# Optimization experiments

Hardware: AMD Instinct MI355X
Metric: run time of the kernel (lower is better)

## Reference

```python
import jax, jax.numpy as jnp
import numpy as np

B, IN, H, OUT, E = 8192, 1024, 4096, 1024, 8
HG = H // 2  # gating hidden

def setup_inputs() -> dict:
    key = jax.random.key(0)
    ks = jax.random.split(key, 9)
    s_in = 1.0 / np.sqrt(IN)
    s_h = 1.0 / np.sqrt(H)
    s_hg = 1.0 / np.sqrt(HG)
    return {
        "x": jax.random.normal(ks[0], (B, IN), jnp.float32),
        # gating MLP: Linear(IN,HG) -> ReLU -> Linear(HG,E) -> softmax
        "gw1": jax.random.uniform(ks[1], (IN, HG), jnp.float32, -s_in, s_in),
        "gb1": jax.random.uniform(ks[2], (HG,), jnp.float32, -s_in, s_in),
        "gw2": jax.random.uniform(ks[3], (HG, E), jnp.float32, -s_hg, s_hg),
        "gb2": jax.random.uniform(ks[4], (E,), jnp.float32, -s_hg, s_hg),
        # experts: E x (Linear(IN,H) -> ReLU -> Linear(H,OUT))
        "ew1": jax.random.uniform(ks[5], (E, IN, H), jnp.float32, -s_in, s_in),
        "eb1": jax.random.uniform(ks[6], (E, H), jnp.float32, -s_in, s_in),
        "ew2": jax.random.uniform(ks[7], (E, H, OUT), jnp.float32, -s_h, s_h),
        "eb2": jax.random.uniform(ks[8], (E, OUT), jnp.float32, -s_h, s_h),
    }

def reference(x, gw1, gb1, gw2, gb2, ew1, eb1, ew2, eb2):
    # Gating network (dropout is a no-op in eval)
    gh = jax.nn.relu(x @ gw1 + gb1)                       # [B, HG]
    gates = jax.nn.softmax(gh @ gw2 + gb2, axis=1)        # [B, E]
    # All experts run on the full batch
    h = jax.nn.relu(jnp.einsum('bi,eih->beh', x, ew1) + eb1[None])  # [B, E, H]
    eo = jnp.einsum('beh,eho->beo', h, ew2) + eb2[None]             # [B, E, OUT]
    # Gate-weighted combine: (stacked * gates[...,None]).sum(dim=1)
    combined = jnp.einsum('beo,be->bo', eo, gates)        # [B, OUT]
    return combined
```

## Files before the change

### kernel.cpp

```cpp
#include <hip/hip_runtime.h>


#define DI __device__ __forceinline__

typedef _Float16 f16;
typedef _Float16 f16x8 __attribute__((ext_vector_type(8)));
typedef float f32x4 __attribute__((ext_vector_type(4)));

constexpr int BSZ  = 8192;
constexpr int IND  = 1024;
constexpr int HID  = 4096;
constexpr int OUTD = 1024;
constexpr int NE   = 8;
constexpr int HGD  = 2048;

__global__ __launch_bounds__(256) void conv_f32_f16_kernel(
    const float* __restrict__ in, f16* __restrict__ out)
{
    size_t i = ((size_t)blockIdx.x * 256 + threadIdx.x) * 8;
    const float4* p = (const float4*)(in + i);
    float4 a = p[0], b = p[1];
    f16x8 v = {(f16)a.x, (f16)a.y, (f16)a.z, (f16)a.w,
               (f16)b.x, (f16)b.y, (f16)b.z, (f16)b.w};
    *(f16x8*)(out + i) = v;
}

__global__ __launch_bounds__(256) void transpose_f32_f16_kernel(
    const float* __restrict__ W, f16* __restrict__ Wt, int K, int N)
{
    __shared__ float t[64][65];
    int n0 = blockIdx.x * 64, k0 = blockIdx.y * 64;
    int tx = threadIdx.x & 63, ty = threadIdx.x >> 6;
#pragma unroll
    for (int i = 0; i < 16; i++) {
        int k = i * 4 + ty;
        t[k][tx] = W[(size_t)(k0 + k) * N + n0 + tx];
    }
    __syncthreads();
#pragma unroll
    for (int i = 0; i < 16; i++) {
        int n = i * 4 + ty;
        Wt[(size_t)(n0 + n) * K + k0 + tx] = (f16)t[tx][n];
    }
}

DI void gload_lds16(const void* g, void* l)
{
    typedef const __attribute__((address_space(1))) unsigned int as1_t;
    typedef __attribute__((address_space(3))) unsigned int as3_t;
    __builtin_amdgcn_global_load_lds(
        (as1_t*)(unsigned long long)(__SIZE_TYPE__)g,
        (as3_t*)(unsigned int)(__SIZE_TYPE__)l,
        16, 0, 0);
}

#define SYNC_HEAD                                                              \
    __builtin_amdgcn_sched_barrier(0);                                         \
    __builtin_amdgcn_s_barrier();                                              \
    asm volatile("s_waitcnt lgkmcnt(0)" ::: "memory");                         \
    __builtin_amdgcn_sched_barrier(0);
#define SYNC_HEAD_T8                                                           \
    __builtin_amdgcn_sched_barrier(0);                                         \
    asm volatile("s_waitcnt lgkmcnt(8)");                                      \
    __builtin_amdgcn_s_barrier();                                              \
    asm volatile("s_waitcnt lgkmcnt(0)" ::: "memory");                         \
    __builtin_amdgcn_sched_barrier(0);
#define SYNC_TAIL                                                              \
    __builtin_amdgcn_sched_barrier(0);                                         \
    __builtin_amdgcn_s_barrier();                                              \
    asm volatile("" ::: "memory");

template <bool RELU>
__global__ __launch_bounds__(512, 2) void gemm256_kernel(
    const f16* __restrict__ A, const f16* __restrict__ Bt,
    const float* __restrict__ bias, f16* __restrict__ Cptr,
    int M, int N, int K)
{
    constexpr int BM = 256, BN = 256, BK = 64;
    constexpr int AT = BM * BK * 2, BT = BN * BK * 2;
    __shared__ __align__(16) f16 sA[2][BM * BK];
    __shared__ __align__(16) f16 sB[2][BN * BK];
    const char* sAc = (const char*)sA;
    const char* sBc = (const char*)sB;

    const int tid = threadIdx.x, wid = tid >> 6, lane = tid & 63;
    const int wm = wid >> 2, wn = wid & 3;
    const int nwg = gridDim.x, bid = blockIdx.x;
    const int wg = (bid & 7) * (nwg >> 3) + (bid >> 3);
    const int gx = N / BN;
    const size_t bm = (size_t)(wg / gx) * BM;
    const size_t bn = (size_t)(wg % gx) * BN;

    f32x4 acc[8][4] = {};

    const int rho  = tid >> 3;
    const int slot = (((tid & 7) << 4) ^ (((tid >> 3) & 7) << 4));
    const f16* pA = A  + (bm + rho) * (size_t)K + (slot >> 1);
    const f16* pB = Bt + (bn + rho) * (size_t)K + (slot >> 1);

    auto stA = [&](int b, int q, int T) {
        gload_lds16(pA + ((size_t)q * 64) * K + (size_t)T * BK,
                    (char*)sAc + b * AT + q * 8192 + wid * 1024);
    };
    auto stB = [&](int b, int q, int T) {
        gload_lds16(pB + ((size_t)q * 64) * K + (size_t)T * BK,
                    (char*)sBc + b * BT + q * 8192 + wid * 1024);
    };

    int offA0[8], offB0[4];
#pragma unroll
    for (int f = 0; f < 8; f++) {
        int r = wm * 128 + f * 16 + (lane & 15);
        offA0[f] = r * 128 + ((((lane >> 4) << 4)) ^ ((r & 7) << 4));
    }
#pragma unroll
    for (int f = 0; f < 4; f++) {
        int r = wn * 64 + f * 16 + (lane & 15);
        offB0[f] = r * 128 + ((((lane >> 4) << 4)) ^ ((r & 7) << 4));
    }

    f16x8 av[4][2], bv0[2][2], bv1[2][2];

#define LDAQ(B, MH)                                                            \
    _Pragma("unroll") for (int f = 0; f < 4; f++)                              \
    _Pragma("unroll") for (int kc = 0; kc < 2; kc++)                           \
        av[f][kc] = *(const f16x8*)(sAc + (B) * AT + (offA0[(MH)*4+f] ^ (kc << 6)));
#define LDBH(B, NH, BV)                                                        \
    _Pragma("unroll") for (int f = 0; f < 2; f++)                              \
    _Pragma("unroll") for (int kc = 0; kc < 2; kc++)                           \
        BV[f][kc] = *(const f16x8*)(sBc + (B) * BT + (offB0[(NH)*2+f] ^ (kc << 6)));
#define QUAD(MH, NH, BV)                                                       \
    __builtin_amdgcn_s_setprio(1);                                             \
    _Pragma("unroll") for (int f = 0; f < 4; f++)                              \
    _Pragma("unroll") for (int g = 0; g < 2; g++)                              \
    _Pragma("unroll") for (int kc = 0; kc < 2; kc++)                           \
        acc[(MH)*4+f][(NH)*2+g] = __builtin_amdgcn_mfma_f32_16x16x32_f16(      \
            av[f][kc], BV[g][kc], acc[(MH)*4+f][(NH)*2+g], 0, 0, 0);           \
    __builtin_amdgcn_s_setprio(0);

    const int NT = K / BK, NI = NT / 2;

    stA(0,0,0); stA(0,2,0); stB(0,0,0); stB(0,1,0); stB(0,2,0); stB(0,3,0);
    stA(0,1,0); stA(0,3,0);
    stA(1,0,1); stA(1,2,1); stB(1,0,1); stB(1,1,1); stB(1,2,1); stB(1,3,1);
    asm volatile("s_waitcnt vmcnt(6)");
    __builtin_amdgcn_s_barrier();
    asm volatile("" ::: "memory");

    for (int i = 0; i < NI - 1; ++i) {
        const int t = 2 * i;
        LDAQ(0, 0) LDBH(0, 0, bv0)
        stA(1, 1, t + 1); stA(1, 3, t + 1);
        SYNC_HEAD_T8
        QUAD(0, 0, bv0)
        SYNC_TAIL
        LDBH(0, 1, bv1)
        stA(0, 0, t + 2); stA(0, 2, t + 2);
        SYNC_HEAD
        QUAD(0, 1, bv1)
        SYNC_TAIL
        LDAQ(0, 1)
        stB(0, 0, t + 2); stB(0, 1, t + 2);
        SYNC_HEAD
        QUAD(1, 1, bv1)
        SYNC_TAIL
        stB(0, 2, t + 2); stB(0, 3, t + 2);
        SYNC_HEAD
        QUAD(1, 0, bv0)
        asm volatile("s_waitcnt vmcnt(6)");
        SYNC_TAIL
        LDAQ(1, 0) LDBH(1, 0, bv0)
        stA(0, 1, t + 2); stA(0, 3, t + 2);
        SYNC_HEAD_T8
        QUAD(0, 0, bv0)
        SYNC_TAIL
        LDBH(1, 1, bv1)
        stA(1, 0, t + 3); stA(1, 2, t + 3);
        SYNC_HEAD
        QUAD(0, 1, bv1)
        SYNC_TAIL
        LDAQ(1, 1)
        stB(1, 0, t + 3); stB(1, 1, t + 3);
        SYNC_HEAD
        QUAD(1, 1, bv1)
        SYNC_TAIL
        stB(1, 2, t + 3); stB(1, 3, t + 3);
        SYNC_HEAD
        QUAD(1, 0, bv0)
        asm volatile("s_waitcnt vmcnt(6)");
        SYNC_TAIL
    }
    {
        LDAQ(0, 0) LDBH(0, 0, bv0)
        stA(1, 1, NT - 1); stA(1, 3, NT - 1);
        SYNC_HEAD_T8
        QUAD(0, 0, bv0)
        SYNC_TAIL
        LDBH(0, 1, bv1)
        SYNC_HEAD
        QUAD(0, 1, bv1)
        SYNC_TAIL
        LDAQ(0, 1)
        SYNC_HEAD
        QUAD(1, 1, bv1)
        SYNC_TAIL
        SYNC_HEAD
        QUAD(1, 0, bv0)
        asm volatile("s_waitcnt vmcnt(0)");
        SYNC_TAIL
        LDAQ(1, 0) LDBH(1, 0, bv0)
        SYNC_HEAD
        QUAD(0, 0, bv0)
        SYNC_TAIL
        LDBH(1, 1, bv1)
        SYNC_HEAD
        QUAD(0, 1, bv1)
        SYNC_TAIL
        LDAQ(1, 1)
        SYNC_HEAD
        QUAD(1, 1, bv1)
        SYNC_TAIL
        SYNC_HEAD
        QUAD(1, 0, bv0)
        SYNC_TAIL
    }
#undef LDAQ
#undef LDBH
#undef QUAD

    const size_t row0 = bm + (size_t)wm * 128;
    const int col0 = (int)bn + wn * 64;
    const int c0 = lane & 15, r0 = (lane >> 4) * 4;
#pragma unroll
    for (int fm = 0; fm < 8; fm++)
#pragma unroll
        for (int r = 0; r < 4; r++) {
            const size_t row = row0 + fm * 16 + r0 + r;
#pragma unroll
            for (int n = 0; n < 4; n++) {
                const size_t col = (size_t)col0 + n * 16 + c0;
                float v = acc[fm][n][r] + bias[col];
                if constexpr (RELU) v = fmaxf(v, 0.0f);
                Cptr[row * (size_t)N + col] = (f16)v;
            }
        }
}

template <bool ACCUM>
__global__ __launch_bounds__(512, 2) void gemmO_kernel(
    const f16* __restrict__ A, const f16* __restrict__ Bt,
    const float* __restrict__ bias, const float* __restrict__ gate,
    float* __restrict__ Cptr, int M, int N, int K)
{
    constexpr int BM = 256, BN = 128, BK = 64;
    constexpr int AT = BM * BK * 2, BT = BN * BK * 2;
    __shared__ __align__(16) f16 sA[2][BM * BK];
    __shared__ __align__(16) f16 sB[2][BN * BK];
    const char* sAc = (const char*)sA;
    const char* sBc = (const char*)sB;

    const int tid = threadIdx.x, wid = tid >> 6, lane = tid & 63;
    const int wm = wid >> 2, wn = wid & 3;
    const int nwg = gridDim.x, bid = blockIdx.x;
    const int wg = (bid & 7) * (nwg >> 3) + (bid >> 3);
    const int gx = N / BN;
    const size_t bm = (size_t)(wg / gx) * BM;
    const size_t bn = (size_t)(wg % gx) * BN;

    f32x4 acc[8][2] = {};

    const int rho  = tid >> 3;
    const int slot = (((tid & 7) << 4) ^ (((tid >> 3) & 7) << 4));
    const f16* pA = A  + (bm + rho) * (size_t)K + (slot >> 1);
    const f16* pB = Bt + (bn + rho) * (size_t)K + (slot >> 1);

    auto stA = [&](int b, int q, int T) {
        gload_lds16(pA + ((size_t)q * 64) * K + (size_t)T * BK,
                    (char*)sAc + b * AT + q * 8192 + wid * 1024);
    };
    auto stB = [&](int b, int q, int T) {
        gload_lds16(pB + ((size_t)q * 64) * K + (size_t)T * BK,
                    (char*)sBc + b * BT + q * 8192 + wid * 1024);
    };

    int offA0[8], offB0[2];
#pragma unroll
    for (int f = 0; f < 8; f++) {
        int r = wm * 128 + f * 16 + (lane & 15);
        offA0[f] = r * 128 + ((((lane >> 4) << 4)) ^ ((r & 7) << 4));
    }
#pragma unroll
    for (int f = 0; f < 2; f++) {
        int r = wn * 32 + f * 16 + (lane & 15);
        offB0[f] = r * 128 + ((((lane >> 4) << 4)) ^ ((r & 7) << 4));
    }

    f16x8 av[4], bv[2][2];

#define LDA4(B, MH, KC)                                                        \
    _Pragma("unroll") for (int f = 0; f < 4; f++)                              \
        av[f] = *(const f16x8*)(sAc + (B) * AT + (offA0[(MH)*4+f] ^ ((KC) << 6)));
#define LDBA(B)                                                                \
    _Pragma("unroll") for (int f = 0; f < 2; f++)                              \
    _Pragma("unroll") for (int kc = 0; kc < 2; kc++)                           \
        bv[f][kc] = *(const f16x8*)(sBc + (B) * BT + (offB0[f] ^ (kc << 6)));
#define OCT(MH, KC)                                                            \
    __builtin_amdgcn_s_setprio(1);                                             \
    _Pragma("unroll") for (int f = 0; f < 4; f++)                              \
    _Pragma("unroll") for (int g = 0; g < 2; g++)                              \
        acc[(MH)*4+f][g] = __builtin_amdgcn_mfma_f32_16x16x32_f16(             \
            av[f], bv[g][KC], acc[(MH)*4+f][g], 0, 0, 0);                      \
    __builtin_amdgcn_s_setprio(0);

    const int NT = K / BK, NI = NT / 2;

    stA(0,0,0); stA(0,2,0); stB(0,0,0); stB(0,1,0); stA(0,1,0); stA(0,3,0);
    stA(1,0,1); stA(1,2,1); stB(1,0,1); stB(1,1,1);
    asm volatile("s_waitcnt vmcnt(4)");
    __builtin_amdgcn_s_barrier();
    asm volatile("" ::: "memory");

    for (int i = 0; i < NI - 1; ++i) {
        const int t = 2 * i;
        LDA4(0, 0, 0) LDBA(0)
        stA(1, 1, t + 1); stA(1, 3, t + 1);
        SYNC_HEAD
        OCT(0, 0)
        SYNC_TAIL
        LDA4(0, 0, 1)
        SYNC_HEAD
        OCT(0, 1)
        SYNC_TAIL
        LDA4(0, 1, 0)
        stA(0, 0, t + 2); stA(0, 2, t + 2);
        SYNC_HEAD
        OCT(1, 0)
        SYNC_TAIL
        LDA4(0, 1, 1)
        stB(0, 0, t + 2); stB(0, 1, t + 2);
        SYNC_HEAD
        OCT(1, 1)
        asm volatile("s_waitcnt vmcnt(4)");
        SYNC_TAIL
        LDA4(1, 0, 0) LDBA(1)
        stA(0, 1, t + 2); stA(0, 3, t + 2);
        SYNC_HEAD
        OCT(0, 0)
        SYNC_TAIL
        LDA4(1, 0, 1)
        SYNC_HEAD
        OCT(0, 1)
        SYNC_TAIL
        LDA4(1, 1, 0)
        stA(1, 0, t + 3); stA(1, 2, t + 3);
        SYNC_HEAD
        OCT(1, 0)
        SYNC_TAIL
        LDA4(1, 1, 1)
        stB(1, 0, t + 3); stB(1, 1, t + 3);
        SYNC_HEAD
        OCT(1, 1)
        asm volatile("s_waitcnt vmcnt(4)");
        SYNC_TAIL
    }
    {
        LDA4(0, 0, 0) LDBA(0)
        stA(1, 1, NT - 1); stA(1, 3, NT - 1);
        SYNC_HEAD
        OCT(0, 0)
        SYNC_TAIL
        LDA4(0, 0, 1)
        SYNC_HEAD
        OCT(0, 1)
        SYNC_TAIL
        LDA4(0, 1, 0)
        SYNC_HEAD
        OCT(1, 0)
        SYNC_TAIL
        LDA4(0, 1, 1)
        SYNC_HEAD
        OCT(1, 1)
        asm volatile("s_waitcnt vmcnt(0)");
        SYNC_TAIL
        LDA4(1, 0, 0) LDBA(1)
        SYNC_HEAD
        OCT(0, 0)
        SYNC_TAIL
        LDA4(1, 0, 1)
        SYNC_HEAD
        OCT(0, 1)
        SYNC_TAIL
        LDA4(1, 1, 0)
        SYNC_HEAD
        OCT(1, 0)
        SYNC_TAIL
        LDA4(1, 1, 1)
        SYNC_HEAD
        OCT(1, 1)
        SYNC_TAIL
    }
#undef LDA4
#undef LDBA
#undef OCT

    const size_t row0 = bm + (size_t)wm * 128;
    const int col0 = (int)bn + wn * 32;
    const int c0 = lane & 15, r0 = (lane >> 4) * 4;
#pragma unroll
    for (int fm = 0; fm < 8; fm++)
#pragma unroll
        for (int r = 0; r < 4; r++) {
            const size_t row = row0 + fm * 16 + r0 + r;
            const float g = gate[row * NE];
#pragma unroll
            for (int n = 0; n < 2; n++) {
                const size_t col = (size_t)col0 + n * 16 + c0;
                float v = (acc[fm][n][r] + bias[col]) * g;
                float* p = Cptr + row * (size_t)N + col;
                *p = ACCUM ? (*p + v) : v;
            }
        }
}

__global__ __launch_bounds__(256) void gate_softmax_kernel(
    const f16* __restrict__ gh, const float* __restrict__ gw2,
    const float* __restrict__ gb2, float* __restrict__ gates)
{
    const int row  = blockIdx.x * 4 + (threadIdx.x >> 6);
    const int lane = threadIdx.x & 63;
    const f16* r = gh + (size_t)row * HGD;
    float acc[NE] = {};
    for (int k = lane; k < HGD; k += 64) {
        float h = (float)r[k];
        const float* w = gw2 + (size_t)k * NE;
#pragma unroll
        for (int e = 0; e < NE; e++) acc[e] = fmaf(h, w[e], acc[e]);
    }
#pragma unroll
    for (int off = 32; off > 0; off >>= 1)
#pragma unroll
        for (int e = 0; e < NE; e++) acc[e] += __shfl_down(acc[e], off, 64);
    if (lane == 0) {
        float l[NE], m = -1e30f;
#pragma unroll
        for (int e = 0; e < NE; e++) { l[e] = acc[e] + gb2[e]; m = fmaxf(m, l[e]); }
        float s = 0.f;
#pragma unroll
        for (int e = 0; e < NE; e++) { l[e] = expf(l[e] - m); s += l[e]; }
        float inv = 1.0f / s;
#pragma unroll
        for (int e = 0; e < NE; e++) gates[(size_t)row * NE + e] = l[e] * inv;
    }
}

extern "C" void kernel_launch(void* const* d_in, const int* in_sizes, int n_in,
                              void* d_out, int out_size, void* d_ws, size_t ws_size,
                              hipStream_t stream)
{
    const float* x   = (const float*)d_in[0];
    const float* gw1 = (const float*)d_in[1];
    const float* gb1 = (const float*)d_in[2];
    const float* gw2 = (const float*)d_in[3];
    const float* gb2 = (const float*)d_in[4];
    const float* ew1 = (const float*)d_in[5];
    const float* eb1 = (const float*)d_in[6];
    const float* ew2 = (const float*)d_in[7];
    const float* eb2 = (const float*)d_in[8];
    float* out = (float*)d_out;

    char* ws = (char*)d_ws;
    float* gates = (float*)ws;
    f16* x16  = (f16*)(ws + (256 << 10));
    f16* wbuf = x16 + (size_t)BSZ * IND;
    f16* hbuf = wbuf + (size_t)HID * IND;
    f16* gh   = hbuf;

    conv_f32_f16_kernel<<<(BSZ * IND) / (256 * 8), 256, 0, stream>>>(x, x16);

    transpose_f32_f16_kernel<<<dim3(HGD / 64, IND / 64), 256, 0, stream>>>(gw1, wbuf, IND, HGD);
    gemm256_kernel<true>
        <<<(HGD / 256) * (BSZ / 256), 512, 0, stream>>>(
            x16, wbuf, gb1, gh, BSZ, HGD, IND);

    gate_softmax_kernel<<<BSZ / 4, 256, 0, stream>>>(gh, gw2, gb2, gates);

    for (int e = 0; e < NE; e++) {
        transpose_f32_f16_kernel<<<dim3(HID / 64, IND / 64), 256, 0, stream>>>(
            ew1 + (size_t)e * IND * HID, wbuf, IND, HID);
        gemm256_kernel<true>
            <<<(HID / 256) * (BSZ / 256), 512, 0, stream>>>(
                x16, wbuf, eb1 + (size_t)e * HID, hbuf, BSZ, HID, IND);

        transpose_f32_f16_kernel<<<dim3(OUTD / 64, HID / 64), 256, 0, stream>>>(
            ew2 + (size_t)e * HID * OUTD, wbuf, HID, OUTD);
        if (e == 0)
            gemmO_kernel<false>
                <<<(OUTD / 128) * (BSZ / 256), 512, 0, stream>>>(
                    hbuf, wbuf, eb2 + (size_t)e * OUTD, gates + e, out, BSZ, OUTD, HID);
        else
            gemmO_kernel<true>
                <<<(OUTD / 128) * (BSZ / 256), 512, 0, stream>>>(
                    hbuf, wbuf, eb2 + (size_t)e * OUTD, gates + e, out, BSZ, OUTD, HID);
    }
}
```

Measured before the change: 1.381 ms.

## Batch all experts into one wide up-projection and one concatenated down-projection GEMM

When the workspace is large enough, all expert W1 matrices are transposed into one concatenated buffer and a single GEMM produces the hidden activations for all experts, with the gate weight folded into the ReLU epilogue. A single down-projection GEMM then contracts over the concatenated E*H dimension, with the gate-weighted bias sum computed in its epilogue. This replaces 16 expert GEMM launches and the read-modify-write accumulation of the fp32 output with two large GEMMs. In exchange it needs a much larger workspace (a B x E*H fp16 hidden buffer), and gate-scaling the activations before the fp16 store changes rounding. The old per-expert path remains as a fallback when the workspace is too small.

```diff
diff --git a/kernel.cpp b/kernel.cpp
--- a/kernel.cpp
+++ b/kernel.cpp
@@ -26,7 +26,8 @@
 }
 
 __global__ __launch_bounds__(256) void transpose_f32_f16_kernel(
-    const float* __restrict__ W, f16* __restrict__ Wt, int K, int N)
+    const float* __restrict__ W, f16* __restrict__ Wt, int K, int N,
+    int ldo, int ko)
 {
     __shared__ float t[64][65];
     int n0 = blockIdx.x * 64, k0 = blockIdx.y * 64;
@@ -40,7 +41,7 @@
 #pragma unroll
     for (int i = 0; i < 16; i++) {
         int n = i * 4 + ty;
-        Wt[(size_t)(n0 + n) * K + k0 + tx] = (f16)t[tx][n];
+        Wt[(size_t)(n0 + n) * ldo + ko + k0 + tx] = (f16)t[tx][n];
     }
 }
 
@@ -70,11 +71,11 @@
     __builtin_amdgcn_s_barrier();                                              \
     asm volatile("" ::: "memory");
 
-template <bool RELU>
+template <bool RELU, bool GSCALE>
 __global__ __launch_bounds__(512, 2) void gemm256_kernel(
     const f16* __restrict__ A, const f16* __restrict__ Bt,
-    const float* __restrict__ bias, f16* __restrict__ Cptr,
-    int M, int N, int K)
+    const float* __restrict__ bias, const float* __restrict__ gate,
+    f16* __restrict__ Cptr, int M, int N, int K)
 {
     constexpr int BM = 256, BN = 256, BK = 64;
     constexpr int AT = BM * BK * 2, BT = BN * BK * 2;
@@ -236,17 +237,20 @@
 #pragma unroll
         for (int r = 0; r < 4; r++) {
             const size_t row = row0 + fm * 16 + r0 + r;
+            float g = 1.0f;
+            if constexpr (GSCALE) g = gate[row * NE + (col0 >> 12)];
 #pragma unroll
             for (int n = 0; n < 4; n++) {
                 const size_t col = (size_t)col0 + n * 16 + c0;
                 float v = acc[fm][n][r] + bias[col];
                 if constexpr (RELU) v = fmaxf(v, 0.0f);
+                if constexpr (GSCALE) v *= g;
                 Cptr[row * (size_t)N + col] = (f16)v;
             }
         }
 }
 
-template <bool ACCUM>
+template <bool ACCUM, bool FUSEBIAS>
 __global__ __launch_bounds__(512, 2) void gemmO_kernel(
     const f16* __restrict__ A, const f16* __restrict__ Bt,
     const float* __restrict__ bias, const float* __restrict__ gate,
@@ -406,20 +410,49 @@
     const size_t row0 = bm + (size_t)wm * 128;
     const int col0 = (int)bn + wn * 32;
     const int c0 = lane & 15, r0 = (lane >> 4) * 4;
-#pragma unroll
-    for (int fm = 0; fm < 8; fm++)
-#pragma unroll
-        for (int r = 0; r < 4; r++) {
-            const size_t row = row0 + fm * 16 + r0 + r;
-            const float g = gate[row * NE];
-#pragma unroll
-            for (int n = 0; n < 2; n++) {
-                const size_t col = (size_t)col0 + n * 16 + c0;
-                float v = (acc[fm][n][r] + bias[col]) * g;
-                float* p = Cptr + row * (size_t)N + col;
-                *p = ACCUM ? (*p + v) : v;
+
+    if constexpr (FUSEBIAS) {
+        float e2[2][NE];
+#pragma unroll
+        for (int n = 0; n < 2; n++) {
+            const int col = col0 + n * 16 + c0;
+#pragma unroll
+            for (int e = 0; e < NE; e++) e2[n][e] = bias[e * OUTD + col];
+        }
+#pragma unroll
+        for (int fm = 0; fm < 8; fm++)
+#pragma unroll
+            for (int r = 0; r < 4; r++) {
+                const size_t row = row0 + fm * 16 + r0 + r;
+                const float* gr = gate + row * NE;
+                float gv[NE];
+#pragma unroll
+                for (int e = 0; e < NE; e++) gv[e] = gr[e];
+#pragma unroll
+                for (int n = 0; n < 2; n++) {
+                    float bb = 0.f;
+#pragma unroll
+                    for (int e = 0; e < NE; e++) bb = fmaf(gv[e], e2[n][e], bb);
+                    const size_t col = (size_t)col0 + n * 16 + c0;
+                    Cptr[row * (size_t)N + col] = acc[fm][n][r] + bb;
+                }
             }
-        }
+    } else {
+#pragma unroll
+        for (int fm = 0; fm < 8; fm++)
+#pragma unroll
+            for (int r = 0; r < 4; r++) {
+                const size_t row = row0 + fm * 16 + r0 + r;
+                const float g = gate[row * NE];
+#pragma unroll
+                for (int n = 0; n < 2; n++) {
+                    const size_t col = (size_t)col0 + n * 16 + c0;
+                    float v = (acc[fm][n][r] + bias[col]) * g;
+                    float* p = Cptr + row * (size_t)N + col;
+                    *p = ACCUM ? (*p + v) : v;
+                }
+            }
+    }
 }
 
 __global__ __launch_bounds__(256) void gate_softmax_kernel(
@@ -468,38 +501,76 @@
     const float* eb2 = (const float*)d_in[8];
     float* out = (float*)d_out;
 
+    constexpr int EH = NE * HID;
+    const size_t need_fused =
+        (size_t)(256 << 10)
+        + (size_t)BSZ * IND * 2
+        + (size_t)OUTD * EH * 2
+        + (size_t)BSZ * EH * 2;
+
     char* ws = (char*)d_ws;
     float* gates = (float*)ws;
-    f16* x16  = (f16*)(ws + (256 << 10));
-    f16* wbuf = x16 + (size_t)BSZ * IND;
-    f16* hbuf = wbuf + (size_t)HID * IND;
-    f16* gh   = hbuf;
+    f16* x16 = (f16*)(ws + (256 << 10));
 
     conv_f32_f16_kernel<<<(BSZ * IND) / (256 * 8), 256, 0, stream>>>(x, x16);
 
-    transpose_f32_f16_kernel<<<dim3(HGD / 64, IND / 64), 256, 0, stream>>>(gw1, wbuf, IND, HGD);
-    gemm256_kernel<true>
-        <<<(HGD / 256) * (BSZ / 256), 512, 0, stream>>>(
-            x16, wbuf, gb1, gh, BSZ, HGD, IND);
-
-    gate_softmax_kernel<<<BSZ / 4, 256, 0, stream>>>(gh, gw2, gb2, gates);
-
-    for (int e = 0; e < NE; e++) {
-        transpose_f32_f16_kernel<<<dim3(HID / 64, IND / 64), 256, 0, stream>>>(
-            ew1 + (size_t)e * IND * HID, wbuf, IND, HID);
-        gemm256_kernel<true>
-            <<<(HID / 256) * (BSZ / 256), 512, 0, stream>>>(
-                x16, wbuf, eb1 + (size_t)e * HID, hbuf, BSZ, HID, IND);
-
-        transpose_f32_f16_kernel<<<dim3(OUTD / 64, HID / 64), 256, 0, stream>>>(
-            ew2 + (size_t)e * HID * OUTD, wbuf, HID, OUTD);
-        if (e == 0)
-            gemmO_kernel<false>
-                <<<(OUTD / 128) * (BSZ / 256), 512, 0, stream>>>(
-                    hbuf, wbuf, eb2 + (size_t)e * OUTD, gates + e, out, BSZ, OUTD, HID);
-        else
-            gemmO_kernel<true>
-                <<<(OUTD / 128) * (BSZ / 256), 512, 0, stream>>>(
-                    hbuf, wbuf, eb2 + (size_t)e * OUTD, gates + e, out, BSZ, OUTD, HID);
-    }
-}
+    if (ws_size >= need_fused) {
+        f16* wcat = x16 + (size_t)BSZ * IND;
+        f16* hs   = wcat + (size_t)OUTD * EH;
+        f16* gh   = hs;
+
+        transpose_f32_f16_kernel<<<dim3(HGD / 64, IND / 64), 256, 0, stream>>>(
+            gw1, wcat, IND, HGD, IND, 0);
+        gemm256_kernel<true, false>
+            <<<(HGD / 256) * (BSZ / 256), 512, 0, stream>>>(
+                x16, wcat, gb1, nullptr, gh, BSZ, HGD, IND);
+        gate_softmax_kernel<<<BSZ / 4, 256, 0, stream>>>(gh, gw2, gb2, gates);
+
+        for (int e = 0; e < NE; e++)
+            transpose_f32_f16_kernel<<<dim3(HID / 64, IND / 64), 256, 0, stream>>>(
+                ew1 + (size_t)e * IND * HID, wcat + (size_t)e * HID * IND,
+                IND, HID, IND, 0);
+        gemm256_kernel<true, true>
+            <<<(EH / 256) * (BSZ / 256), 512, 0, stream>>>(
+                x16, wcat, eb1, gates, hs, BSZ, EH, IND);
+
+        for (int e = 0; e < NE; e++)
+            transpose_f32_f16_kernel<<<dim3(OUTD / 64, HID / 64), 256, 0, stream>>>(
+                ew2 + (size_t)e * HID * OUTD, wcat, HID, OUTD, EH, e * HID);
+        gemmO_kernel<false, true>
+            <<<(OUTD / 128) * (BSZ / 256), 512, 0, stream>>>(
+                hs, wcat, eb2, gates, out, BSZ, OUTD, EH);
+    } else {
+        f16* wbuf = x16 + (size_t)BSZ * IND;
+        f16* hbuf = wbuf + (size_t)HID * IND;
+        f16* gh   = hbuf;
+
+        transpose_f32_f16_kernel<<<dim3(HGD / 64, IND / 64), 256, 0, stream>>>(
+            gw1, wbuf, IND, HGD, IND, 0);
+        gemm256_kernel<true, false>
+            <<<(HGD / 256) * (BSZ / 256), 512, 0, stream>>>(
+                x16, wbuf, gb1, nullptr, gh, BSZ, HGD, IND);
+        gate_softmax_kernel<<<BSZ / 4, 256, 0, stream>>>(gh, gw2, gb2, gates);
+
+        for (int e = 0; e < NE; e++) {
+            transpose_f32_f16_kernel<<<dim3(HID / 64, IND / 64), 256, 0, stream>>>(
+                ew1 + (size_t)e * IND * HID, wbuf, IND, HID, IND, 0);
+            gemm256_kernel<true, false>
+                <<<(HID / 256) * (BSZ / 256), 512, 0, stream>>>(
+                    x16, wbuf, eb1 + (size_t)e * HID, nullptr, hbuf, BSZ, HID, IND);
+
+            transpose_f32_f16_kernel<<<dim3(OUTD / 64, HID / 64), 256, 0, stream>>>(
+                ew2 + (size_t)e * HID * OUTD, wbuf, HID, OUTD, HID, 0);
+            if (e == 0)
+                gemmO_kernel<false, false>
+                    <<<(OUTD / 128) * (BSZ / 256), 512, 0, stream>>>(
+                        hbuf, wbuf, eb2 + (size_t)e * OUTD, gates + e, out,
+                        BSZ, OUTD, HID);
+            else
+                gemmO_kernel<true, false>
+                    <<<(OUTD / 128) * (BSZ / 256), 512, 0, stream>>>(
+                        hbuf, wbuf, eb2 + (size_t)e * OUTD, gates + e, out,
+                        BSZ, OUTD, HID);
+        }
+    }
+}
```

New measurement: 1.382 ms. About the same (+0.1%).

## Replace output GEMM with 128x128 tile, 4-stage pipelined kernel

Applied to the files above, without the earlier changes.

Replaces the second expert GEMM (hidden to output, with gate-weighted accumulate) with a new kernel that uses 128x128 tiles, BK=32 and 256 threads. It uses a 4-deep LDS ring buffer with register double-buffering, so MFMAs overlap the LDS reads and global prefetches. The aim is better latency hiding and higher occupancy on the K=4096 GEMM. In exchange, each block reuses less data, so per-FLOP LDS and global traffic rises and the grid doubles. The transpose kernel also gains output stride and offset parameters, but every call currently passes values that reproduce the old behaviour.

```diff
diff --git a/kernel.cpp b/kernel.cpp
--- a/kernel.cpp
+++ b/kernel.cpp
@@ -26,7 +26,8 @@
 }
 
 __global__ __launch_bounds__(256) void transpose_f32_f16_kernel(
-    const float* __restrict__ W, f16* __restrict__ Wt, int K, int N)
+    const float* __restrict__ W, f16* __restrict__ Wt, int K, int N,
+    int ldo, int ko)
 {
     __shared__ float t[64][65];
     int n0 = blockIdx.x * 64, k0 = blockIdx.y * 64;
@@ -40,7 +41,7 @@
 #pragma unroll
     for (int i = 0; i < 16; i++) {
         int n = i * 4 + ty;
-        Wt[(size_t)(n0 + n) * K + k0 + tx] = (f16)t[tx][n];
+        Wt[(size_t)(n0 + n) * ldo + ko + k0 + tx] = (f16)t[tx][n];
     }
 }
 
@@ -246,176 +247,140 @@
         }
 }
 
+
+#define STGO(BB, TT) { stA(BB, 0, TT); stA(BB, 1, TT);                         \
+                       stB(BB, 0, TT); stB(BB, 1, TT); }
+
+#define RDO(B, RS)                                                             \
+    _Pragma("unroll") for (int f = 0; f < 4; f++) {                            \
+        av##RS[f] = *(const f16x8*)(sAc + (B) * 8192 + offA[f]);               \
+        bv##RS[f] = *(const f16x8*)(sBc + (B) * 8192 + offB[f]);               \
+    }
+
+#define MMO(MS)                                                                \
+    __builtin_amdgcn_s_setprio(1);                                             \
+    _Pragma("unroll") for (int fa = 0; fa < 4; fa++)                           \
+    _Pragma("unroll") for (int fb = 0; fb < 4; fb++)                           \
+        acc[fa][fb] = __builtin_amdgcn_mfma_f32_16x16x32_f16(                  \
+            av##MS[fa], bv##MS[fb], acc[fa][fb], 0, 0, 0);                     \
+    __builtin_amdgcn_s_setprio(0);
+
+#define PHO_FULL(T, B, RS, MS)                                                 \
+  {                                                                            \
+    STGO(((B) + 3) & 3, (T) + 3)                                               \
+    asm volatile("s_waitcnt vmcnt(8)");                                        \
+    __builtin_amdgcn_sched_barrier(0);                                         \
+    __builtin_amdgcn_s_barrier();                                              \
+    asm volatile("" ::: "memory");                                             \
+    RDO(((B) + 1) & 3, RS)                                                     \
+    __builtin_amdgcn_sched_barrier(0);                                         \
+    MMO(MS)                                                                    \
+    asm volatile("s_waitcnt lgkmcnt(0)" ::: "memory");                         \
+    __builtin_amdgcn_sched_barrier(0);                                         \
+  }
+
+#define PHO_TAIL(B, RS, MS, VM)                                                \
+  {                                                                            \
+    asm volatile("s_waitcnt vmcnt(" #VM ")");                                  \
+    __builtin_amdgcn_sched_barrier(0);                                         \
+    __builtin_amdgcn_s_barrier();                                              \
+    asm volatile("" ::: "memory");                                             \
+    RDO(((B) + 1) & 3, RS)                                                     \
+    __builtin_amdgcn_sched_barrier(0);                                         \
+    MMO(MS)                                                                    \
+    asm volatile("s_waitcnt lgkmcnt(0)" ::: "memory");                         \
+    __builtin_amdgcn_sched_barrier(0);                                         \
+  }
+
 template <bool ACCUM>
-__global__ __launch_bounds__(512, 2) void gemmO_kernel(
+__global__ __launch_bounds__(256, 2) void gemmO2_kernel(
     const f16* __restrict__ A, const f16* __restrict__ Bt,
     const float* __restrict__ bias, const float* __restrict__ gate,
     float* __restrict__ Cptr, int M, int N, int K)
 {
-    constexpr int BM = 256, BN = 128, BK = 64;
-    constexpr int AT = BM * BK * 2, BT = BN * BK * 2;
-    __shared__ __align__(16) f16 sA[2][BM * BK];
-    __shared__ __align__(16) f16 sB[2][BN * BK];
+    constexpr int BM = 128, BN = 128, BK = 32;
+    __shared__ __align__(16) f16 sA[4][BM * BK];
+    __shared__ __align__(16) f16 sB[4][BN * BK];
     const char* sAc = (const char*)sA;
     const char* sBc = (const char*)sB;
 
     const int tid = threadIdx.x, wid = tid >> 6, lane = tid & 63;
-    const int wm = wid >> 2, wn = wid & 3;
+    const int wm = wid >> 1, wn = wid & 1;
+
     const int nwg = gridDim.x, bid = blockIdx.x;
     const int wg = (bid & 7) * (nwg >> 3) + (bid >> 3);
     const int gx = N / BN;
     const size_t bm = (size_t)(wg / gx) * BM;
     const size_t bn = (size_t)(wg % gx) * BN;
 
-    f32x4 acc[8][2] = {};
-
-    const int rho  = tid >> 3;
-    const int slot = (((tid & 7) << 4) ^ (((tid >> 3) & 7) << 4));
-    const f16* pA = A  + (bm + rho) * (size_t)K + (slot >> 1);
-    const f16* pB = Bt + (bn + rho) * (size_t)K + (slot >> 1);
+    f32x4 acc[4][4] = {};
+
+    const int sl  = (tid & 7) ^ ((tid >> 3) & 7);
+    const int r0s = ((tid >> 3) << 1) + (sl >> 2);
+    const int kel = (sl & 3) * 8;
+    const f16* pA = A  + (bm + r0s) * (size_t)K + kel;
+    const f16* pB = Bt + (bn + r0s) * (size_t)K + kel;
 
     auto stA = [&](int b, int q, int T) {
         gload_lds16(pA + ((size_t)q * 64) * K + (size_t)T * BK,
-                    (char*)sAc + b * AT + q * 8192 + wid * 1024);
+                    (char*)sAc + b * 8192 + q * 4096 + wid * 1024);
     };
     auto stB = [&](int b, int q, int T) {
         gload_lds16(pB + ((size_t)q * 64) * K + (size_t)T * BK,
-                    (char*)sBc + b * BT + q * 8192 + wid * 1024);
+                    (char*)sBc + b * 8192 + q * 4096 + wid * 1024);
     };
 
-    int offA0[8], offB0[2];
-#pragma unroll
-    for (int f = 0; f < 8; f++) {
-        int r = wm * 128 + f * 16 + (lane & 15);
-        offA0[f] = r * 128 + ((((lane >> 4) << 4)) ^ ((r & 7) << 4));
-    }
-#pragma unroll
-    for (int f = 0; f < 2; f++) {
-        int r = wn * 32 + f * 16 + (lane & 15);
-        offB0[f] = r * 128 + ((((lane >> 4) << 4)) ^ ((r & 7) << 4));
-    }
-
-    f16x8 av[4], bv[2][2];
-
-#define LDA4(B, MH, KC)                                                        \
-    _Pragma("unroll") for (int f = 0; f < 4; f++)                              \
-        av[f] = *(const f16x8*)(sAc + (B) * AT + (offA0[(MH)*4+f] ^ ((KC) << 6)));
-#define LDBA(B)                                                                \
-    _Pragma("unroll") for (int f = 0; f < 2; f++)                              \
-    _Pragma("unroll") for (int kc = 0; kc < 2; kc++)                           \
-        bv[f][kc] = *(const f16x8*)(sBc + (B) * BT + (offB0[f] ^ (kc << 6)));
-#define OCT(MH, KC)                                                            \
-    __builtin_amdgcn_s_setprio(1);                                             \
-    _Pragma("unroll") for (int f = 0; f < 4; f++)                              \
-    _Pragma("unroll") for (int g = 0; g < 2; g++)                              \
-        acc[(MH)*4+f][g] = __builtin_amdgcn_mfma_f32_16x16x32_f16(             \
-            av[f], bv[g][KC], acc[(MH)*4+f][g], 0, 0, 0);                      \
-    __builtin_amdgcn_s_setprio(0);
-
-    const int NT = K / BK, NI = NT / 2;
-
-    stA(0,0,0); stA(0,2,0); stB(0,0,0); stB(0,1,0); stA(0,1,0); stA(0,3,0);
-    stA(1,0,1); stA(1,2,1); stB(1,0,1); stB(1,1,1);
-    asm volatile("s_waitcnt vmcnt(4)");
+    int offA[4], offB[4];
+    const int ks = lane >> 4;
+#pragma unroll
+    for (int f = 0; f < 4; f++) {
+        int r = wm * 64 + f * 16 + (lane & 15);
+        int P = r >> 1;
+        offA[f] = P * 128 + ((((r & 1) << 2) | ks) ^ (P & 7)) * 16;
+        r = wn * 64 + f * 16 + (lane & 15);
+        P = r >> 1;
+        offB[f] = P * 128 + ((((r & 1) << 2) | ks) ^ (P & 7)) * 16;
+    }
+
+    f16x8 av0[4], bv0[4], av1[4], bv1[4];
+    const int NT = K / BK;
+
+    STGO(0, 0) STGO(1, 1) STGO(2, 2)
+    asm volatile("s_waitcnt vmcnt(8)");
     __builtin_amdgcn_s_barrier();
     asm volatile("" ::: "memory");
-
-    for (int i = 0; i < NI - 1; ++i) {
-        const int t = 2 * i;
-        LDA4(0, 0, 0) LDBA(0)
-        stA(1, 1, t + 1); stA(1, 3, t + 1);
-        SYNC_HEAD
-        OCT(0, 0)
-        SYNC_TAIL
-        LDA4(0, 0, 1)
-        SYNC_HEAD
-        OCT(0, 1)
-        SYNC_TAIL
-        LDA4(0, 1, 0)
-        stA(0, 0, t + 2); stA(0, 2, t + 2);
-        SYNC_HEAD
-        OCT(1, 0)
-        SYNC_TAIL
-        LDA4(0, 1, 1)
-        stB(0, 0, t + 2); stB(0, 1, t + 2);
-        SYNC_HEAD
-        OCT(1, 1)
-        asm volatile("s_waitcnt vmcnt(4)");
-        SYNC_TAIL
-        LDA4(1, 0, 0) LDBA(1)
-        stA(0, 1, t + 2); stA(0, 3, t + 2);
-        SYNC_HEAD
-        OCT(0, 0)
-        SYNC_TAIL
-        LDA4(1, 0, 1)
-        SYNC_HEAD
-        OCT(0, 1)
-        SYNC_TAIL
-        LDA4(1, 1, 0)
-        stA(1, 0, t + 3); stA(1, 2, t + 3);
-        SYNC_HEAD
-        OCT(1, 0)
-        SYNC_TAIL
-        LDA4(1, 1, 1)
-        stB(1, 0, t + 3); stB(1, 1, t + 3);
-        SYNC_HEAD
-        OCT(1, 1)
-        asm volatile("s_waitcnt vmcnt(4)");
-        SYNC_TAIL
-    }
+    RDO(0, 0)
+    asm volatile("s_waitcnt lgkmcnt(0)" ::: "memory");
+    __builtin_amdgcn_sched_barrier(0);
+
+    for (int t = 0; t < NT - 4; t += 4) {
+        PHO_FULL(t + 0, 0, 1, 0)
+        PHO_FULL(t + 1, 1, 0, 1)
+        PHO_FULL(t + 2, 2, 1, 0)
+        PHO_FULL(t + 3, 3, 0, 1)
+    }
+    PHO_FULL(NT - 4, 0, 1, 0)
+    PHO_TAIL(1, 0, 1, 4)
+    PHO_TAIL(2, 1, 0, 0)
     {
-        LDA4(0, 0, 0) LDBA(0)
-        stA(1, 1, NT - 1); stA(1, 3, NT - 1);
-        SYNC_HEAD
-        OCT(0, 0)
-        SYNC_TAIL
-        LDA4(0, 0, 1)
-        SYNC_HEAD
-        OCT(0, 1)
-        SYNC_TAIL
-        LDA4(0, 1, 0)
-        SYNC_HEAD
-        OCT(1, 0)
-        SYNC_TAIL
-        LDA4(0, 1, 1)
-        SYNC_HEAD
-        OCT(1, 1)
-        asm volatile("s_waitcnt vmcnt(0)");
-        SYNC_TAIL
-        LDA4(1, 0, 0) LDBA(1)
-        SYNC_HEAD
-        OCT(0, 0)
-        SYNC_TAIL
-        LDA4(1, 0, 1)
-        SYNC_HEAD
-        OCT(0, 1)
-        SYNC_TAIL
-        LDA4(1, 1, 0)
-        SYNC_HEAD
-        OCT(1, 0)
-        SYNC_TAIL
-        LDA4(1, 1, 1)
-        SYNC_HEAD
-        OCT(1, 1)
-        SYNC_TAIL
-    }
-#undef LDA4
-#undef LDBA
-#undef OCT
-
-    const size_t row0 = bm + (size_t)wm * 128;
-    const int col0 = (int)bn + wn * 32;
+        __builtin_amdgcn_s_barrier();
+        asm volatile("" ::: "memory");
+        MMO(1)
+    }
+
+    const size_t row0 = bm + (size_t)wm * 64;
+    const int col0 = (int)bn + wn * 64;
     const int c0 = lane & 15, r0 = (lane >> 4) * 4;
 #pragma unroll
-    for (int fm = 0; fm < 8; fm++)
+    for (int fa = 0; fa < 4; fa++)
 #pragma unroll
         for (int r = 0; r < 4; r++) {
-            const size_t row = row0 + fm * 16 + r0 + r;
+            const size_t row = row0 + fa * 16 + r0 + r;
             const float g = gate[row * NE];
 #pragma unroll
-            for (int n = 0; n < 2; n++) {
-                const size_t col = (size_t)col0 + n * 16 + c0;
-                float v = (acc[fm][n][r] + bias[col]) * g;
+            for (int fb = 0; fb < 4; fb++) {
+                const size_t col = (size_t)col0 + fb * 16 + c0;
+                float v = (acc[fa][fb][r] + bias[col]) * g;
                 float* p = Cptr + row * (size_t)N + col;
                 *p = ACCUM ? (*p + v) : v;
             }
@@ -477,7 +442,8 @@
 
     conv_f32_f16_kernel<<<(BSZ * IND) / (256 * 8), 256, 0, stream>>>(x, x16);
 
-    transpose_f32_f16_kernel<<<dim3(HGD / 64, IND / 64), 256, 0, stream>>>(gw1, wbuf, IND, HGD);
+    transpose_f32_f16_kernel<<<dim3(HGD / 64, IND / 64), 256, 0, stream>>>(
+        gw1, wbuf, IND, HGD, IND, 0);
     gemm256_kernel<true>
         <<<(HGD / 256) * (BSZ / 256), 512, 0, stream>>>(
             x16, wbuf, gb1, gh, BSZ, HGD, IND);
@@ -486,20 +452,22 @@
 
     for (int e = 0; e < NE; e++) {
         transpose_f32_f16_kernel<<<dim3(HID / 64, IND / 64), 256, 0, stream>>>(
-            ew1 + (size_t)e * IND * HID, wbuf, IND, HID);
+            ew1 + (size_t)e * IND * HID, wbuf, IND, HID, IND, 0);
         gemm256_kernel<true>
             <<<(HID / 256) * (BSZ / 256), 512, 0, stream>>>(
                 x16, wbuf, eb1 + (size_t)e * HID, hbuf, BSZ, HID, IND);
 
         transpose_f32_f16_kernel<<<dim3(OUTD / 64, HID / 64), 256, 0, stream>>>(
-            ew2 + (size_t)e * HID * OUTD, wbuf, HID, OUTD);
+            ew2 + (size_t)e * HID * OUTD, wbuf, HID, OUTD, HID, 0);
         if (e == 0)
-            gemmO_kernel<false>
-                <<<(OUTD / 128) * (BSZ / 256), 512, 0, stream>>>(
-                    hbuf, wbuf, eb2 + (size_t)e * OUTD, gates + e, out, BSZ, OUTD, HID);
+            gemmO2_kernel<false>
+                <<<(OUTD / 128) * (BSZ / 128), 256, 0, stream>>>(
+                    hbuf, wbuf, eb2 + (size_t)e * OUTD, gates + e, out,
+                    BSZ, OUTD, HID);
         else
-            gemmO_kernel<true>
-                <<<(OUTD / 128) * (BSZ / 256), 512, 0, stream>>>(
-                    hbuf, wbuf, eb2 + (size_t)e * OUTD, gates + e, out, BSZ, OUTD, HID);
-    }
-}
+            gemmO2_kernel<true>
+                <<<(OUTD / 128) * (BSZ / 128), 256, 0, stream>>>(
+                    hbuf, wbuf, eb2 + (size_t)e * OUTD, gates + e, out,
+                    BSZ, OUTD, HID);
+    }
+}
```

Result: slower. 1.459 ms (+5.7%).

## Switch GEMM kernels from 16x16x32 to 32x32x16 MFMA tiles

Applied to the files above, without the earlier changes.

Both GEMM kernels now use the 32x32x16 f16 MFMA instruction with 16-register accumulators instead of 16x16x32, and the LDS fragment addressing and epilogue row/column mapping are reworked to match. Larger MFMA tiles mean fewer LDS reads per flop and fewer instructions issued. The gating softmax kernel also loads 8 f16 values per vector read instead of scalar loads. The cost is a changed epilogue store pattern and possible LDS bank-conflict shifts under the existing swizzle.

```diff
diff --git a/kernel.cpp b/kernel.cpp
--- a/kernel.cpp
+++ b/kernel.cpp
@@ -5,7 +5,7 @@
 
 typedef _Float16 f16;
 typedef _Float16 f16x8 __attribute__((ext_vector_type(8)));
-typedef float f32x4 __attribute__((ext_vector_type(4)));
+typedef float f32x16 __attribute__((ext_vector_type(16)));
 
 constexpr int BSZ  = 8192;
 constexpr int IND  = 1024;
@@ -91,7 +91,7 @@
     const size_t bm = (size_t)(wg / gx) * BM;
     const size_t bn = (size_t)(wg % gx) * BN;
 
-    f32x4 acc[8][4] = {};
+    f32x16 acc[4][2] = {};
 
     const int rho  = tid >> 3;
     const int slot = (((tid & 7) << 4) ^ (((tid >> 3) & 7) << 4));
@@ -107,35 +107,33 @@
                     (char*)sBc + b * BT + q * 8192 + wid * 1024);
     };
 
-    int offA0[8], offB0[4];
-#pragma unroll
-    for (int f = 0; f < 8; f++) {
-        int r = wm * 128 + f * 16 + (lane & 15);
-        offA0[f] = r * 128 + ((((lane >> 4) << 4)) ^ ((r & 7) << 4));
-    }
+    int offA[4], offB0v[2];
 #pragma unroll
     for (int f = 0; f < 4; f++) {
-        int r = wn * 64 + f * 16 + (lane & 15);
-        offB0[f] = r * 128 + ((((lane >> 4) << 4)) ^ ((r & 7) << 4));
-    }
-
-    f16x8 av[4][2], bv0[2][2], bv1[2][2];
+        int r = wm * 128 + f * 32 + (lane & 31);
+        offA[f] = r * 128 + ((((lane >> 5) << 4)) ^ ((r & 7) << 4));
+    }
+#pragma unroll
+    for (int f = 0; f < 2; f++) {
+        int r = wn * 64 + f * 32 + (lane & 31);
+        offB0v[f] = r * 128 + ((((lane >> 5) << 4)) ^ ((r & 7) << 4));
+    }
+
+    f16x8 av[2][4], bv0[4], bv1[4];
 
 #define LDAQ(B, MH)                                                            \
-    _Pragma("unroll") for (int f = 0; f < 4; f++)                              \
-    _Pragma("unroll") for (int kc = 0; kc < 2; kc++)                           \
-        av[f][kc] = *(const f16x8*)(sAc + (B) * AT + (offA0[(MH)*4+f] ^ (kc << 6)));
+    _Pragma("unroll") for (int f = 0; f < 2; f++)                              \
+    _Pragma("unroll") for (int ks = 0; ks < 4; ks++)                           \
+        av[f][ks] = *(const f16x8*)(sAc + (B) * AT + (offA[(MH)*2+f] ^ (ks << 5)));
 #define LDBH(B, NH, BV)                                                        \
-    _Pragma("unroll") for (int f = 0; f < 2; f++)                              \
-    _Pragma("unroll") for (int kc = 0; kc < 2; kc++)                           \
-        BV[f][kc] = *(const f16x8*)(sBc + (B) * BT + (offB0[(NH)*2+f] ^ (kc << 6)));
+    _Pragma("unroll") for (int ks = 0; ks < 4; ks++)                           \
+        BV[ks] = *(const f16x8*)(sBc + (B) * BT + (offB0v[NH] ^ (ks << 5)));
 #define QUAD(MH, NH, BV)                                                       \
     __builtin_amdgcn_s_setprio(1);                                             \
-    _Pragma("unroll") for (int f = 0; f < 4; f++)                              \
-    _Pragma("unroll") for (int g = 0; g < 2; g++)                              \
-    _Pragma("unroll") for (int kc = 0; kc < 2; kc++)                           \
-        acc[(MH)*4+f][(NH)*2+g] = __builtin_amdgcn_mfma_f32_16x16x32_f16(      \
-            av[f][kc], BV[g][kc], acc[(MH)*4+f][(NH)*2+g], 0, 0, 0);           \
+    _Pragma("unroll") for (int f = 0; f < 2; f++)                              \
+    _Pragma("unroll") for (int ks = 0; ks < 4; ks++)                           \
+        acc[(MH)*2+f][NH] = __builtin_amdgcn_mfma_f32_32x32x16_f16(            \
+            av[f][ks], BV[ks], acc[(MH)*2+f][NH], 0, 0, 0);                    \
     __builtin_amdgcn_s_setprio(0);
 
     const int NT = K / BK, NI = NT / 2;
@@ -230,16 +228,16 @@
 
     const size_t row0 = bm + (size_t)wm * 128;
     const int col0 = (int)bn + wn * 64;
-    const int c0 = lane & 15, r0 = (lane >> 4) * 4;
-#pragma unroll
-    for (int fm = 0; fm < 8; fm++)
-#pragma unroll
-        for (int r = 0; r < 4; r++) {
-            const size_t row = row0 + fm * 16 + r0 + r;
-#pragma unroll
-            for (int n = 0; n < 4; n++) {
-                const size_t col = (size_t)col0 + n * 16 + c0;
-                float v = acc[fm][n][r] + bias[col];
+    const int c0 = lane & 31, rhi = 4 * (lane >> 5);
+#pragma unroll
+    for (int fm = 0; fm < 4; fm++)
+#pragma unroll
+        for (int reg = 0; reg < 16; reg++) {
+            const size_t row = row0 + fm * 32 + (reg & 3) + 8 * (reg >> 2) + rhi;
+#pragma unroll
+            for (int fn = 0; fn < 2; fn++) {
+                const size_t col = (size_t)col0 + fn * 32 + c0;
+                float v = acc[fm][fn][reg] + bias[col];
                 if constexpr (RELU) v = fmaxf(v, 0.0f);
                 Cptr[row * (size_t)N + col] = (f16)v;
             }
@@ -267,7 +265,7 @@
     const size_t bm = (size_t)(wg / gx) * BM;
     const size_t bn = (size_t)(wg % gx) * BN;
 
-    f32x4 acc[8][2] = {};
+    f32x16 acc[4] = {};
 
     const int rho  = tid >> 3;
     const int slot = (((tid & 7) << 4) ^ (((tid >> 3) & 7) << 4));
@@ -283,33 +281,33 @@
                     (char*)sBc + b * BT + q * 8192 + wid * 1024);
     };
 
-    int offA0[8], offB0[2];
-#pragma unroll
-    for (int f = 0; f < 8; f++) {
-        int r = wm * 128 + f * 16 + (lane & 15);
-        offA0[f] = r * 128 + ((((lane >> 4) << 4)) ^ ((r & 7) << 4));
-    }
-#pragma unroll
-    for (int f = 0; f < 2; f++) {
-        int r = wn * 32 + f * 16 + (lane & 15);
-        offB0[f] = r * 128 + ((((lane >> 4) << 4)) ^ ((r & 7) << 4));
-    }
-
-    f16x8 av[4], bv[2][2];
-
-#define LDA4(B, MH, KC)                                                        \
-    _Pragma("unroll") for (int f = 0; f < 4; f++)                              \
-        av[f] = *(const f16x8*)(sAc + (B) * AT + (offA0[(MH)*4+f] ^ ((KC) << 6)));
+    int offA[4], offB0;
+#pragma unroll
+    for (int f = 0; f < 4; f++) {
+        int r = wm * 128 + f * 32 + (lane & 31);
+        offA[f] = r * 128 + ((((lane >> 5) << 4)) ^ ((r & 7) << 4));
+    }
+    {
+        int r = wn * 32 + (lane & 31);
+        offB0 = r * 128 + ((((lane >> 5) << 4)) ^ ((r & 7) << 4));
+    }
+
+    f16x8 av[2][2], bv[4];
+
+#define LDA2(B, MH, KH)                                                        \
+    _Pragma("unroll") for (int f = 0; f < 2; f++)                              \
+    _Pragma("unroll") for (int j = 0; j < 2; j++)                              \
+        av[f][j] = *(const f16x8*)(sAc + (B) * AT +                            \
+                                   (offA[(MH)*2+f] ^ (((KH)*2+j) << 5)));
 #define LDBA(B)                                                                \
+    _Pragma("unroll") for (int ks = 0; ks < 4; ks++)                           \
+        bv[ks] = *(const f16x8*)(sBc + (B) * BT + (offB0 ^ (ks << 5)));
+#define OCT(MH, KH)                                                            \
+    __builtin_amdgcn_s_setprio(1);                                             \
     _Pragma("unroll") for (int f = 0; f < 2; f++)                              \
-    _Pragma("unroll") for (int kc = 0; kc < 2; kc++)                           \
-        bv[f][kc] = *(const f16x8*)(sBc + (B) * BT + (offB0[f] ^ (kc << 6)));
-#define OCT(MH, KC)                                                            \
-    __builtin_amdgcn_s_setprio(1);                                             \
-    _Pragma("unroll") for (int f = 0; f < 4; f++)                              \
-    _Pragma("unroll") for (int g = 0; g < 2; g++)                              \
-        acc[(MH)*4+f][g] = __builtin_amdgcn_mfma_f32_16x16x32_f16(             \
-            av[f], bv[g][KC], acc[(MH)*4+f][g], 0, 0, 0);                      \
+    _Pragma("unroll") for (int j = 0; j < 2; j++)                              \
+        acc[(MH)*2+f] = __builtin_amdgcn_mfma_f32_32x32x16_f16(                \
+            av[f][j], bv[(KH)*2+j], acc[(MH)*2+f], 0, 0, 0);                   \
     __builtin_amdgcn_s_setprio(0);
 
     const int NT = K / BK, NI = NT / 2;
@@ -322,41 +320,41 @@
 
     for (int i = 0; i < NI - 1; ++i) {
         const int t = 2 * i;
-        LDA4(0, 0, 0) LDBA(0)
+        LDA2(0, 0, 0) LDBA(0)
         stA(1, 1, t + 1); stA(1, 3, t + 1);
         SYNC_HEAD
         OCT(0, 0)
         SYNC_TAIL
-        LDA4(0, 0, 1)
+        LDA2(0, 0, 1)
         SYNC_HEAD
         OCT(0, 1)
         SYNC_TAIL
-        LDA4(0, 1, 0)
+        LDA2(0, 1, 0)
         stA(0, 0, t + 2); stA(0, 2, t + 2);
         SYNC_HEAD
         OCT(1, 0)
         SYNC_TAIL
-        LDA4(0, 1, 1)
+        LDA2(0, 1, 1)
         stB(0, 0, t + 2); stB(0, 1, t + 2);
         SYNC_HEAD
         OCT(1, 1)
         asm volatile("s_waitcnt vmcnt(4)");
         SYNC_TAIL
-        LDA4(1, 0, 0) LDBA(1)
+        LDA2(1, 0, 0) LDBA(1)
         stA(0, 1, t + 2); stA(0, 3, t + 2);
         SYNC_HEAD
         OCT(0, 0)
         SYNC_TAIL
-        LDA4(1, 0, 1)
+        LDA2(1, 0, 1)
         SYNC_HEAD
         OCT(0, 1)
         SYNC_TAIL
-        LDA4(1, 1, 0)
+        LDA2(1, 1, 0)
         stA(1, 0, t + 3); stA(1, 2, t + 3);
         SYNC_HEAD
         OCT(1, 0)
         SYNC_TAIL
-        LDA4(1, 1, 1)
+        LDA2(1, 1, 1)
         stB(1, 0, t + 3); stB(1, 1, t + 3);
         SYNC_HEAD
         OCT(1, 1)
@@ -364,61 +362,58 @@
         SYNC_TAIL
     }
     {
-        LDA4(0, 0, 0) LDBA(0)
+        LDA2(0, 0, 0) LDBA(0)
         stA(1, 1, NT - 1); stA(1, 3, NT - 1);
         SYNC_HEAD
         OCT(0, 0)
         SYNC_TAIL
-        LDA4(0, 0, 1)
+        LDA2(0, 0, 1)
         SYNC_HEAD
         OCT(0, 1)
         SYNC_TAIL
-        LDA4(0, 1, 0)
+        LDA2(0, 1, 0)
         SYNC_HEAD
         OCT(1, 0)
         SYNC_TAIL
-        LDA4(0, 1, 1)
+        LDA2(0, 1, 1)
         SYNC_HEAD
         OCT(1, 1)
         asm volatile("s_waitcnt vmcnt(0)");
         SYNC_TAIL
-        LDA4(1, 0, 0) LDBA(1)
+        LDA2(1, 0, 0) LDBA(1)
         SYNC_HEAD
         OCT(0, 0)
         SYNC_TAIL
-        LDA4(1, 0, 1)
+        LDA2(1, 0, 1)
         SYNC_HEAD
         OCT(0, 1)
         SYNC_TAIL
-        LDA4(1, 1, 0)
+        LDA2(1, 1, 0)
         SYNC_HEAD
         OCT(1, 0)
         SYNC_TAIL
-        LDA4(1, 1, 1)
+        LDA2(1, 1, 1)
         SYNC_HEAD
         OCT(1, 1)
         SYNC_TAIL
     }
-#undef LDA4
+#undef LDA2
 #undef LDBA
 #undef OCT
 
     const size_t row0 = bm + (size_t)wm * 128;
     const int col0 = (int)bn + wn * 32;
-    const int c0 = lane & 15, r0 = (lane >> 4) * 4;
-#pragma unroll
-    for (int fm = 0; fm < 8; fm++)
-#pragma unroll
-        for (int r = 0; r < 4; r++) {
-            const size_t row = row0 + fm * 16 + r0 + r;
+    const int c0 = lane & 31, rhi = 4 * (lane >> 5);
+#pragma unroll
+    for (int fm = 0; fm < 4; fm++)
+#pragma unroll
+        for (int reg = 0; reg < 16; reg++) {
+            const size_t row = row0 + fm * 32 + (reg & 3) + 8 * (reg >> 2) + rhi;
             const float g = gate[row * NE];
-#pragma unroll
-            for (int n = 0; n < 2; n++) {
-                const size_t col = (size_t)col0 + n * 16 + c0;
-                float v = (acc[fm][n][r] + bias[col]) * g;
-                float* p = Cptr + row * (size_t)N + col;
-                *p = ACCUM ? (*p + v) : v;
-            }
+            const size_t col = (size_t)col0 + c0;
+            float v = (acc[fm][reg] + bias[col]) * g;
+            float* p = Cptr + row * (size_t)N + col;
+            *p = ACCUM ? (*p + v) : v;
         }
 }
 
@@ -430,11 +425,15 @@
     const int lane = threadIdx.x & 63;
     const f16* r = gh + (size_t)row * HGD;
     float acc[NE] = {};
-    for (int k = lane; k < HGD; k += 64) {
-        float h = (float)r[k];
-        const float* w = gw2 + (size_t)k * NE;
-#pragma unroll
-        for (int e = 0; e < NE; e++) acc[e] = fmaf(h, w[e], acc[e]);
+    for (int kb = lane * 8; kb < HGD; kb += 512) {
+        f16x8 v = *(const f16x8*)(r + kb);
+#pragma unroll
+        for (int j = 0; j < 8; j++) {
+            float h = (float)v[j];
+            const float* w = gw2 + (size_t)(kb + j) * NE;
+#pragma unroll
+            for (int e = 0; e < NE; e++) acc[e] = fmaf(h, w[e], acc[e]);
+        }
     }
 #pragma unroll
     for (int off = 32; off > 0; off >>= 1)
@@ -477,7 +476,8 @@
 
     conv_f32_f16_kernel<<<(BSZ * IND) / (256 * 8), 256, 0, stream>>>(x, x16);
 
-    transpose_f32_f16_kernel<<<dim3(HGD / 64, IND / 64), 256, 0, stream>>>(gw1, wbuf, IND, HGD);
+    transpose_f32_f16_kernel<<<dim3(HGD / 64, IND / 64), 256, 0, stream>>>(
+        gw1, wbuf, IND, HGD);
     gemm256_kernel<true>
         <<<(HGD / 256) * (BSZ / 256), 512, 0, stream>>>(
             x16, wbuf, gb1, gh, BSZ, HGD, IND);
@@ -496,10 +496,12 @@
         if (e == 0)
             gemmO_kernel<false>
                 <<<(OUTD / 128) * (BSZ / 256), 512, 0, stream>>>(
-                    hbuf, wbuf, eb2 + (size_t)e * OUTD, gates + e, out, BSZ, OUTD, HID);
+                    hbuf, wbuf, eb2 + (size_t)e * OUTD, gates + e, out,
+                    BSZ, OUTD, HID);
         else
             gemmO_kernel<true>
                 <<<(OUTD / 128) * (BSZ / 256), 512, 0, stream>>>(
-                    hbuf, wbuf, eb2 + (size_t)e * OUTD, gates + e, out, BSZ, OUTD, HID);
-    }
-}
+                    hbuf, wbuf, eb2 + (size_t)e * OUTD, gates + e, out,
+                    BSZ, OUTD, HID);
+    }
+}
```

New measurement: 1.587 ms. 1.15x slower.
